# Kernel optimization log

Measured on AMD Instinct MI355X. Metric: run time of the kernel, lower is better.

Reference implementation:

```python
import jax, jax.numpy as jnp
import numpy as np

N_NODES = 100000
N_EDGES = 1600000
D_FEAT = 128


def setup_inputs() -> dict:
    key = jax.random.key(0)
    k1, k2, k3 = jax.random.split(key, 3)
    feat = jax.random.normal(k1, (N_NODES, D_FEAT), dtype=jnp.float32)
    src = jax.random.randint(k2, (N_EDGES,), 0, N_NODES, dtype=jnp.int32)
    dst = jax.random.randint(k3, (N_EDGES,), 0, N_NODES, dtype=jnp.int32)
    return {"feat": feat, "src": src, "dst": dst}


def reference(feat, src, dst):
    n = feat.shape[0]
    ones = jnp.ones(src.shape[0], dtype=feat.dtype)
    # out-degree of each node (as message source), clamped to >= 1
    deg_o = jnp.clip(jax.ops.segment_sum(ones, src, num_segments=n), 1.0)
    norm_l = deg_o ** -0.5  # [N]
    feat_scaled = feat * norm_l[:, None]
    # copy_u + sum aggregation: gather from src, scatter-add to dst
    agg = jax.ops.segment_sum(feat_scaled[src], dst, num_segments=n)
    # in-degree normalization on destination side
    deg_i = jnp.clip(jax.ops.segment_sum(ones, dst, num_segments=n), 1.0)
    norm_r = deg_i ** -0.5
    return agg * norm_r[:, None]
```

## Files before the change

### kernel.cpp

```cpp
#include <hip/hip_runtime.h>
#include <hip/hip_fp16.h>

#define D_FEAT      128
#define S_BIN       256
#define BUCKET_BITS 7
#define BUCKET_SZ   128
#define NB_MAX      1024
#define SORT_CAP    6144
#define BIGB        1024

typedef float f32x4 __attribute__((ext_vector_type(4)));

__global__ __launch_bounds__(BIGB) void binhist2_kernel(
        const int* __restrict__ src, const int* __restrict__ dst,
        int* __restrict__ part2, int n_edges, int nb, int N2, int slice_len) {
    __shared__ int hd[NB_MAX];
    __shared__ int hs[NB_MAX];
    int s = blockIdx.x, tid = threadIdx.x;
    for (int i = tid; i < nb; i += BIGB) { hd[i] = 0; hs[i] = 0; }
    __syncthreads();
    int beg = s * slice_len;
    int end = beg + slice_len; if (end > n_edges) end = n_edges;
    for (int i = beg + tid; i < end; i += BIGB) {
        atomicAdd(&hd[dst[i] >> BUCKET_BITS], 1);
        atomicAdd(&hs[src[i] >> BUCKET_BITS], 1);
    }
    __syncthreads();
    for (int b = tid; b < nb; b += BIGB) {
        part2[(size_t)b * S_BIN + s] = hd[b];
        part2[(size_t)(N2 + b * S_BIN) + s] = hs[b];
    }
}

__global__ __launch_bounds__(BIGB) void scan1_kernel(int* __restrict__ data,
        int* __restrict__ bsum, int n) {
    __shared__ int wsum[16];
    int tid = threadIdx.x;
    int g = blockIdx.x * BIGB + tid;
    int lane = tid & 63, w = tid >> 6;
    int v = (g < n) ? data[g] : 0;
    int incl = v;
    #pragma unroll
    for (int d = 1; d < 64; d <<= 1) {
        int x = __shfl_up(incl, d, 64);
        if (lane >= d) incl += x;
    }
    if (lane == 63) wsum[w] = incl;
    __syncthreads();
    if (w == 0) {
        int sv = (lane < 16) ? wsum[lane] : 0;
        #pragma unroll
        for (int d = 1; d < 16; d <<= 1) {
            int x = __shfl_up(sv, d, 64);
            if (lane >= d) sv += x;
        }
        if (lane < 16) wsum[lane] = sv;
    }
    __syncthreads();
    int wpre = (w > 0) ? wsum[w - 1] : 0;
    if (g < n) data[g] = wpre + incl - v;
    if (tid == BIGB - 1) bsum[blockIdx.x] = wpre + incl;
}

__global__ __launch_bounds__(BIGB) void scan2_kernel(int* __restrict__ bsum, int nchunks) {
    __shared__ int wsum[16];
    int tid = threadIdx.x;
    int lane = tid & 63, w = tid >> 6;
    int v = (tid < nchunks) ? bsum[tid] : 0;
    int incl = v;
    #pragma unroll
    for (int d = 1; d < 64; d <<= 1) {
        int x = __shfl_up(incl, d, 64);
        if (lane >= d) incl += x;
    }
    if (lane == 63) wsum[w] = incl;
    __syncthreads();
    if (w == 0) {
        int sv = (lane < 16) ? wsum[lane] : 0;
        #pragma unroll
        for (int d = 1; d < 16; d <<= 1) {
            int x = __shfl_up(sv, d, 64);
            if (lane >= d) sv += x;
        }
        if (lane < 16) wsum[lane] = sv;
    }
    __syncthreads();
    int wpre = (w > 0) ? wsum[w - 1] : 0;
    if (tid < nchunks) bsum[tid] = wpre + incl - v;
}

__global__ __launch_bounds__(BIGB) void binscatter2_kernel(
        const int* __restrict__ src, const int* __restrict__ dst,
        const int* __restrict__ loff, const int* __restrict__ bsum,
        int* __restrict__ colp, unsigned char* __restrict__ colp_src,
        int n_edges, int nb, int N2, int slice_len) {
    __shared__ int cd[NB_MAX];
    __shared__ int cs[NB_MAX];
    int s = blockIdx.x, tid = threadIdx.x;
    for (int b = tid; b < nb; b += BIGB) {
        size_t iD = (size_t)b * S_BIN + s;
        size_t iS = (size_t)N2 + (size_t)b * S_BIN + s;
        cd[b] = loff[iD] + bsum[iD >> 10];
        cs[b] = loff[iS] + bsum[iS >> 10] - n_edges;
    }
    __syncthreads();
    int beg = s * slice_len;
    int end = beg + slice_len; if (end > n_edges) end = n_edges;
    for (int i = beg + tid; i < end; i += BIGB) {
        int d = dst[i], sv = src[i];
        int pD = atomicAdd(&cd[d >> BUCKET_BITS], 1);
        colp[pD] = sv | ((d & (BUCKET_SZ - 1)) << 20);
        int pS = atomicAdd(&cs[sv >> BUCKET_BITS], 1);
        colp_src[pS] = (unsigned char)(sv & (BUCKET_SZ - 1));
    }
}

__global__ __launch_bounds__(256) void sortcount_kernel(
        int* __restrict__ colp, const unsigned char* __restrict__ colp_src,
        const int* __restrict__ loff, const int* __restrict__ bsum,
        int* __restrict__ node_off, float* __restrict__ norm_l,
        int n_nodes, int n_edges, int nb, int N2) {
    __shared__ int buf[SORT_CAP];
    __shared__ int cnt[BUCKET_SZ];
    __shared__ int sa[BUCKET_SZ];
    __shared__ int sb[BUCKET_SZ];
    int tid = threadIdx.x;

    if ((int)blockIdx.x >= nb) {
        int b = blockIdx.x - nb;
        size_t iA = (size_t)N2 + (size_t)b * S_BIN;
        int beg = loff[iA] + bsum[iA >> 10] - n_edges;
        int end;
        if (b + 1 < nb) {
            size_t iB = (size_t)N2 + (size_t)(b + 1) * S_BIN;
            end = loff[iB] + bsum[iB >> 10] - n_edges;
        } else end = n_edges;
        if (tid < BUCKET_SZ) cnt[tid] = 0;
        __syncthreads();
        for (int i = beg + tid; i < end; i += blockDim.x)
            atomicAdd(&cnt[colp_src[i]], 1);
        __syncthreads();
        int node0 = b << BUCKET_BITS;
        int bn = n_nodes - node0; if (bn > BUCKET_SZ) bn = BUCKET_SZ;
        if (tid < bn) {
            int c = cnt[tid]; if (c < 1) c = 1;
            norm_l[node0 + tid] = rsqrtf((float)c);
        }
        return;
    }

    int b = blockIdx.x;
    size_t iA = (size_t)b * S_BIN;
    int beg = loff[iA] + bsum[iA >> 10];
    int end;
    if (b + 1 < nb) {
        size_t iB = (size_t)(b + 1) * S_BIN;
        end = loff[iB] + bsum[iB >> 10];
    } else end = n_edges;
    int m = end - beg;
    if (tid < BUCKET_SZ) cnt[tid] = 0;
    __syncthreads();
    for (int i = tid; i < m; i += blockDim.x) {
        int v = colp[beg + i];
        if (i < SORT_CAP) buf[i] = v;
        atomicAdd(&cnt[(v >> 20) & (BUCKET_SZ - 1)], 1);
    }
    __syncthreads();
    int* rp = sa; int* wp = sb;
    if (tid < BUCKET_SZ) sa[tid] = cnt[tid];
    __syncthreads();
    for (int d = 1; d < BUCKET_SZ; d <<= 1) {
        if (tid < BUCKET_SZ) wp[tid] = rp[tid] + (tid >= d ? rp[tid - d] : 0);
        __syncthreads();
        int* t = rp; rp = wp; wp = t;
    }
    int node0 = b << BUCKET_BITS;
    int bn = n_nodes - node0; if (bn > BUCKET_SZ) bn = BUCKET_SZ;
    if (tid < BUCKET_SZ) {
        int ex = rp[tid] - cnt[tid];
        wp[tid] = ex;
        if (tid < bn) node_off[node0 + tid] = beg + ex;
    }
    if (b == nb - 1 && tid == 0) node_off[n_nodes] = end;
    __syncthreads();
    int mm = m < SORT_CAP ? m : SORT_CAP;
    for (int i = tid; i < mm; i += blockDim.x) {
        int v = buf[i];
        int p = atomicAdd(&wp[(v >> 20) & (BUCKET_SZ - 1)], 1);
        colp[beg + p] = v & 0xFFFFF;
    }
}

__global__ void convert_kernel(const float* __restrict__ feat, const float* __restrict__ norm_l,
                               __half* __restrict__ feat16, int n_nodes) {
    int t = blockIdx.x * blockDim.x + threadIdx.x;
    int total = n_nodes * (D_FEAT / 8);
    if (t >= total) return;
    float nl = norm_l[t >> 4];
    const f32x4* fp = (const f32x4*)feat + (size_t)t * 2;
    f32x4 a = __builtin_nontemporal_load(fp);
    f32x4 b = __builtin_nontemporal_load(fp + 1);
    __half2 h0 = __floats2half2_rn(a.x * nl, a.y * nl);
    __half2 h1 = __floats2half2_rn(a.z * nl, a.w * nl);
    __half2 h2 = __floats2half2_rn(b.x * nl, b.y * nl);
    __half2 h3 = __floats2half2_rn(b.z * nl, b.w * nl);
    uint4 o;
    o.x = *(unsigned int*)&h0; o.y = *(unsigned int*)&h1;
    o.z = *(unsigned int*)&h2; o.w = *(unsigned int*)&h3;
    ((uint4*)feat16)[t] = o;
}

__global__ __launch_bounds__(256) void pull_csr_kernel(
        const __half* __restrict__ feat16, const int* __restrict__ col,
        const int* __restrict__ node_off, float* __restrict__ out,
        int n_nodes, int n_edges) {
    int lane = threadIdx.x & 63;
    int wid  = (int)(((long long)blockIdx.x * blockDim.x + threadIdx.x) >> 6);
    int h  = lane >> 5;
    int g  = (lane >> 4) & 1;
    int dl = lane & 15;
    int node = wid * 2 + h;
    bool nvalid = node < n_nodes;
    int nsafe = nvalid ? node : n_nodes - 1;
    int s = node_off[nsafe];
    int e = nvalid ? node_off[nsafe + 1] : s;
    int m = e - s;
    int om = __shfl_xor(m, 32, 64);
    int mm = m > om ? m : om;

    float a0=0.f,a1=0.f,a2=0.f,a3=0.f,a4=0.f,a5=0.f,a6=0.f,a7=0.f;
    const uint4* rowb = (const uint4*)feat16;

    for (int base = 0; base < mm; base += 32) {
        int remh = m - base;
        int ci = lane & 31;
        if (ci >= remh) ci = (remh > 0) ? remh - 1 : 0;
        int cidx = s + base + ci;
        if (cidx >= n_edges) cidx = n_edges - 1;
        int cv = col[cidx];
        int lim = mm - base; if (lim > 32) lim = 32;
        for (int k = 0; k < lim; k += 2) {
            int srcl = (lane & 32) + k + g;
            int idx = __shfl(cv, srcl, 64);
            uint4 hv = rowb[((size_t)(unsigned)idx << 4) + dl];
            float wm = (base + k + g < m) ? 1.f : 0.f;
            float2 f;
            f = __half22float2(*(__half2*)&hv.x); a0 += wm * f.x; a1 += wm * f.y;
            f = __half22float2(*(__half2*)&hv.y); a2 += wm * f.x; a3 += wm * f.y;
            f = __half22float2(*(__half2*)&hv.z); a4 += wm * f.x; a5 += wm * f.y;
            f = __half22float2(*(__half2*)&hv.w); a6 += wm * f.x; a7 += wm * f.y;
        }
    }

    a0 += __shfl_xor(a0, 16, 64); a1 += __shfl_xor(a1, 16, 64);
    a2 += __shfl_xor(a2, 16, 64); a3 += __shfl_xor(a3, 16, 64);
    a4 += __shfl_xor(a4, 16, 64); a5 += __shfl_xor(a5, 16, 64);
    a6 += __shfl_xor(a6, 16, 64); a7 += __shfl_xor(a7, 16, 64);

    if (nvalid && g == 0) {
        int c = m < 1 ? 1 : m;
        float nr = rsqrtf((float)c);
        f32x4 o0 = {a0 * nr, a1 * nr, a2 * nr, a3 * nr};
        f32x4 o1 = {a4 * nr, a5 * nr, a6 * nr, a7 * nr};
        f32x4* op = (f32x4*)(out + (size_t)node * D_FEAT) + dl * 2;
        __builtin_nontemporal_store(o0, op);
        __builtin_nontemporal_store(o1, op + 1);
    }
}

extern "C" void kernel_launch(void* const* d_in, const int* in_sizes, int n_in,
                              void* d_out, int out_size, void* d_ws, size_t ws_size,
                              hipStream_t stream) {
    const float* feat = (const float*)d_in[0];
    const int*   src  = (const int*)d_in[1];
    const int*   dst  = (const int*)d_in[2];
    float* out = (float*)d_out;

    int n_nodes = in_sizes[0] / D_FEAT;
    int n_edges = in_sizes[1];
    int nb = (n_nodes + BUCKET_SZ - 1) / BUCKET_SZ;
    int N2 = nb * S_BIN;
    int NSCAN = 2 * N2;
    int sl = (n_edges + S_BIN - 1) / S_BIN;

    auto alignup = [](size_t x) { return (x + 255) & ~(size_t)255; };
    char* p = (char*)d_ws;
    int*    node_off = (int*)p;            p += alignup((size_t)(n_nodes + 1) * 4);
    float*  norm_l   = (float*)p;          p += alignup((size_t)n_nodes * 4);
    int*    part2    = (int*)p;            p += alignup((size_t)NSCAN * 4);
    int*    bsum     = (int*)p;            p += alignup((size_t)BIGB * 4);
    int*    colp     = (int*)p;            p += alignup((size_t)n_edges * 4);
    unsigned char* colp_src = (unsigned char*)p; p += alignup((size_t)n_edges);
    __half* feat16   = (__half*)p;

    binhist2_kernel<<<S_BIN, BIGB, 0, stream>>>(src, dst, part2, n_edges, nb, N2, sl);

    {
        int nch = (NSCAN + BIGB - 1) / BIGB;
        scan1_kernel<<<nch, BIGB, 0, stream>>>(part2, bsum, NSCAN);
        scan2_kernel<<<1, BIGB, 0, stream>>>(bsum, nch);
    }

    binscatter2_kernel<<<S_BIN, BIGB, 0, stream>>>(src, dst, part2, bsum, colp, colp_src,
                                                   n_edges, nb, N2, sl);

    sortcount_kernel<<<2 * nb, 256, 0, stream>>>(colp, colp_src, part2, bsum, node_off,
                                                 norm_l, n_nodes, n_edges, nb, N2);

    {
        int total = n_nodes * (D_FEAT / 8);
        convert_kernel<<<(total + 255) / 256, 256, 0, stream>>>(feat, norm_l, feat16, n_nodes);
    }

    {
        long long waves = ((long long)n_nodes + 1) / 2;
        long long total = waves * 64;
        pull_csr_kernel<<<(int)((total + 255) / 256), 256, 0, stream>>>(feat16, colp, node_off,
                                                                        out, n_nodes, n_edges);
    }
}
```

Baseline: 227.6 us.

## Fuse scan passes via last-block ticket and fold conversion into sort kernel

Merges the two scan kernels into one, using an atomic ticket so the last finishing block scans the block sums, and folds the fp16 feature conversion into the source-degree branch of the sort kernel, which drops the norm_l buffer. The sort kernel also goes from 256 to 512 threads per block. This removes two kernel launches and a global round trip for norm_l. In exchange the conversion now runs on only ~782 blocks with per-row strided work, which may lower memory parallelism, and the scan relies on threadfence/atomic ordering.

```diff
diff --git a/kernel.cpp b/kernel.cpp
--- a/kernel.cpp
+++ b/kernel.cpp
@@ -13,10 +13,12 @@
 
 __global__ __launch_bounds__(BIGB) void binhist2_kernel(
         const int* __restrict__ src, const int* __restrict__ dst,
-        int* __restrict__ part2, int n_edges, int nb, int N2, int slice_len) {
+        int* __restrict__ part2, int* __restrict__ tick,
+        int n_edges, int nb, int N2, int slice_len) {
     __shared__ int hd[NB_MAX];
     __shared__ int hs[NB_MAX];
     int s = blockIdx.x, tid = threadIdx.x;
+    if (s == 0 && tid == 0) *tick = 0;
     for (int i = tid; i < nb; i += BIGB) { hd[i] = 0; hs[i] = 0; }
     __syncthreads();
     int beg = s * slice_len;
@@ -32,9 +34,10 @@
     }
 }
 
-__global__ __launch_bounds__(BIGB) void scan1_kernel(int* __restrict__ data,
-        int* __restrict__ bsum, int n) {
+__global__ __launch_bounds__(BIGB) void scan_kernel(int* __restrict__ data,
+        int* __restrict__ bsum, int* __restrict__ tick, int n, int nch) {
     __shared__ int wsum[16];
+    __shared__ int amLast;
     int tid = threadIdx.x;
     int g = blockIdx.x * BIGB + tid;
     int lane = tid & 63, w = tid >> 6;
@@ -59,21 +62,23 @@
     __syncthreads();
     int wpre = (w > 0) ? wsum[w - 1] : 0;
     if (g < n) data[g] = wpre + incl - v;
-    if (tid == BIGB - 1) bsum[blockIdx.x] = wpre + incl;
-}
-
-__global__ __launch_bounds__(BIGB) void scan2_kernel(int* __restrict__ bsum, int nchunks) {
-    __shared__ int wsum[16];
-    int tid = threadIdx.x;
-    int lane = tid & 63, w = tid >> 6;
-    int v = (tid < nchunks) ? bsum[tid] : 0;
-    int incl = v;
+    if (tid == BIGB - 1) {
+        bsum[blockIdx.x] = wpre + incl;
+        __threadfence();
+        amLast = (atomicAdd(tick, 1) == (int)gridDim.x - 1);
+    }
+    __syncthreads();
+    if (!amLast) return;
+    __threadfence();
+    int v2 = (tid < nch) ? bsum[tid] : 0;
+    int incl2 = v2;
     #pragma unroll
     for (int d = 1; d < 64; d <<= 1) {
-        int x = __shfl_up(incl, d, 64);
-        if (lane >= d) incl += x;
-    }
-    if (lane == 63) wsum[w] = incl;
+        int x = __shfl_up(incl2, d, 64);
+        if (lane >= d) incl2 += x;
+    }
+    __syncthreads();
+    if (lane == 63) wsum[w] = incl2;
     __syncthreads();
     if (w == 0) {
         int sv = (lane < 16) ? wsum[lane] : 0;
@@ -85,8 +90,8 @@
         if (lane < 16) wsum[lane] = sv;
     }
     __syncthreads();
-    int wpre = (w > 0) ? wsum[w - 1] : 0;
-    if (tid < nchunks) bsum[tid] = wpre + incl - v;
+    int wpre2 = (w > 0) ? wsum[w - 1] : 0;
+    if (tid < nch) bsum[tid] = wpre2 + incl2 - v2;
 }
 
 __global__ __launch_bounds__(BIGB) void binscatter2_kernel(
@@ -115,16 +120,18 @@
     }
 }
 
-__global__ __launch_bounds__(256) void sortcount_kernel(
+__global__ __launch_bounds__(512) void sortconv_kernel(
         int* __restrict__ colp, const unsigned char* __restrict__ colp_src,
         const int* __restrict__ loff, const int* __restrict__ bsum,
-        int* __restrict__ node_off, float* __restrict__ norm_l,
-        int n_nodes, int n_edges, int nb, int N2) {
+        int* __restrict__ node_off, const float* __restrict__ feat,
+        __half* __restrict__ feat16, int n_nodes, int n_edges, int nb, int N2) {
     __shared__ int buf[SORT_CAP];
     __shared__ int cnt[BUCKET_SZ];
     __shared__ int sa[BUCKET_SZ];
     __shared__ int sb[BUCKET_SZ];
+    __shared__ float snl[BUCKET_SZ];
     int tid = threadIdx.x;
+    const int NT = 512;
 
     if ((int)blockIdx.x >= nb) {
         int b = blockIdx.x - nb;
@@ -137,14 +144,31 @@
         } else end = n_edges;
         if (tid < BUCKET_SZ) cnt[tid] = 0;
         __syncthreads();
-        for (int i = beg + tid; i < end; i += blockDim.x)
+        for (int i = beg + tid; i < end; i += NT)
             atomicAdd(&cnt[colp_src[i]], 1);
         __syncthreads();
         int node0 = b << BUCKET_BITS;
         int bn = n_nodes - node0; if (bn > BUCKET_SZ) bn = BUCKET_SZ;
-        if (tid < bn) {
+        if (tid < BUCKET_SZ) {
             int c = cnt[tid]; if (c < 1) c = 1;
-            norm_l[node0 + tid] = rsqrtf((float)c);
+            snl[tid] = rsqrtf((float)c);
+        }
+        __syncthreads();
+        int total = bn * (D_FEAT / 8);
+        for (int i = tid; i < total; i += NT) {
+            int row = i >> 4, q = i & 15;
+            float nl = snl[row];
+            const f32x4* fp = (const f32x4*)(feat + (size_t)(node0 + row) * D_FEAT) + q * 2;
+            f32x4 a = __builtin_nontemporal_load(fp);
+            f32x4 bv = __builtin_nontemporal_load(fp + 1);
+            __half2 h0 = __floats2half2_rn(a.x * nl, a.y * nl);
+            __half2 h1 = __floats2half2_rn(a.z * nl, a.w * nl);
+            __half2 h2 = __floats2half2_rn(bv.x * nl, bv.y * nl);
+            __half2 h3 = __floats2half2_rn(bv.z * nl, bv.w * nl);
+            uint4 o;
+            o.x = *(unsigned int*)&h0; o.y = *(unsigned int*)&h1;
+            o.z = *(unsigned int*)&h2; o.w = *(unsigned int*)&h3;
+            ((uint4*)(feat16 + (size_t)(node0 + row) * D_FEAT))[q] = o;
         }
         return;
     }
@@ -160,7 +184,7 @@
     int m = end - beg;
     if (tid < BUCKET_SZ) cnt[tid] = 0;
     __syncthreads();
-    for (int i = tid; i < m; i += blockDim.x) {
+    for (int i = tid; i < m; i += NT) {
         int v = colp[beg + i];
         if (i < SORT_CAP) buf[i] = v;
         atomicAdd(&cnt[(v >> 20) & (BUCKET_SZ - 1)], 1);
@@ -184,30 +208,11 @@
     if (b == nb - 1 && tid == 0) node_off[n_nodes] = end;
     __syncthreads();
     int mm = m < SORT_CAP ? m : SORT_CAP;
-    for (int i = tid; i < mm; i += blockDim.x) {
+    for (int i = tid; i < mm; i += NT) {
         int v = buf[i];
         int p = atomicAdd(&wp[(v >> 20) & (BUCKET_SZ - 1)], 1);
         colp[beg + p] = v & 0xFFFFF;
     }
-}
-
-__global__ void convert_kernel(const float* __restrict__ feat, const float* __restrict__ norm_l,
-                               __half* __restrict__ feat16, int n_nodes) {
-    int t = blockIdx.x * blockDim.x + threadIdx.x;
-    int total = n_nodes * (D_FEAT / 8);
-    if (t >= total) return;
-    float nl = norm_l[t >> 4];
-    const f32x4* fp = (const f32x4*)feat + (size_t)t * 2;
-    f32x4 a = __builtin_nontemporal_load(fp);
-    f32x4 b = __builtin_nontemporal_load(fp + 1);
-    __half2 h0 = __floats2half2_rn(a.x * nl, a.y * nl);
-    __half2 h1 = __floats2half2_rn(a.z * nl, a.w * nl);
-    __half2 h2 = __floats2half2_rn(b.x * nl, b.y * nl);
-    __half2 h3 = __floats2half2_rn(b.z * nl, b.w * nl);
-    uint4 o;
-    o.x = *(unsigned int*)&h0; o.y = *(unsigned int*)&h1;
-    o.z = *(unsigned int*)&h2; o.w = *(unsigned int*)&h3;
-    ((uint4*)feat16)[t] = o;
 }
 
 __global__ __launch_bounds__(256) void pull_csr_kernel(
@@ -286,31 +291,25 @@
     auto alignup = [](size_t x) { return (x + 255) & ~(size_t)255; };
     char* p = (char*)d_ws;
     int*    node_off = (int*)p;            p += alignup((size_t)(n_nodes + 1) * 4);
-    float*  norm_l   = (float*)p;          p += alignup((size_t)n_nodes * 4);
     int*    part2    = (int*)p;            p += alignup((size_t)NSCAN * 4);
-    int*    bsum     = (int*)p;            p += alignup((size_t)BIGB * 4);
+    int*    bsum     = (int*)p;            p += alignup((size_t)(BIGB + 1) * 4);
+    int*    tick     = bsum + BIGB;
     int*    colp     = (int*)p;            p += alignup((size_t)n_edges * 4);
     unsigned char* colp_src = (unsigned char*)p; p += alignup((size_t)n_edges);
     __half* feat16   = (__half*)p;
 
-    binhist2_kernel<<<S_BIN, BIGB, 0, stream>>>(src, dst, part2, n_edges, nb, N2, sl);
+    binhist2_kernel<<<S_BIN, BIGB, 0, stream>>>(src, dst, part2, tick, n_edges, nb, N2, sl);
 
     {
         int nch = (NSCAN + BIGB - 1) / BIGB;
-        scan1_kernel<<<nch, BIGB, 0, stream>>>(part2, bsum, NSCAN);
-        scan2_kernel<<<1, BIGB, 0, stream>>>(bsum, nch);
+        scan_kernel<<<nch, BIGB, 0, stream>>>(part2, bsum, tick, NSCAN, nch);
     }
 
     binscatter2_kernel<<<S_BIN, BIGB, 0, stream>>>(src, dst, part2, bsum, colp, colp_src,
                                                    n_edges, nb, N2, sl);
 
-    sortcount_kernel<<<2 * nb, 256, 0, stream>>>(colp, colp_src, part2, bsum, node_off,
-                                                 norm_l, n_nodes, n_edges, nb, N2);
-
-    {
-        int total = n_nodes * (D_FEAT / 8);
-        convert_kernel<<<(total + 255) / 256, 256, 0, stream>>>(feat, norm_l, feat16, n_nodes);
-    }
+    sortconv_kernel<<<2 * nb, 512, 0, stream>>>(colp, colp_src, part2, bsum, node_off,
+                                                feat, feat16, n_nodes, n_edges, nb, N2);
 
     {
         long long waves = ((long long)n_nodes + 1) / 2;
```

Result: slower. 236.8 us (+4.1%).
